# Kernel tuning notes

Hardware: AMD Instinct MI355X
Metric: run time of the kernel (lower is better)

Reference implementation:

```python
import jax, jax.numpy as jnp
import numpy as np

B, N, H, DQK, DV = 2, 2048, 16, 128, 128
E = H * DV
CHUNK = 64


def setup_inputs() -> dict:
    key = jax.random.key(0)
    ks = jax.random.split(key, 11)
    w = lambda k: jax.random.normal(k, (E, E), jnp.float32) * 0.02
    return {
        "x": jax.random.normal(ks[0], (B, N, E), jnp.float32),
        "prev_state": jnp.zeros((B, H, DQK, DV), jnp.float32),
        "Wq": w(ks[1]), "bq": jnp.zeros((E,), jnp.float32),
        "Wk": w(ks[2]), "bk": jnp.zeros((E,), jnp.float32),
        "Wv": w(ks[3]), "bv": jnp.zeros((E,), jnp.float32),
        "Wg": w(ks[4]), "bg": jnp.zeros((E,), jnp.float32),
        "Wo": w(ks[5]), "bo": jnp.zeros((E,), jnp.float32),
        "start_idx": 0,
    }


def _mul_i(t):
    # multiply interleaved complex pairs by i: (a, b) -> (-b, a)
    t2 = t.reshape(*t.shape[:-1], -1, 2)
    return jnp.stack((-t2[..., 1], t2[..., 0]), axis=-1).reshape(t.shape)


def reference(x, prev_state, Wq, bq, Wk, bk, Wv, bv, Wg, bg, Wo, bo, start_idx):
    b, n, e = x.shape
    h, dqk, dv, c = H, DQK, DV, CHUNK
    q = (x @ Wq.T + bq).reshape(b, n, h, dqk)
    k = (x @ Wk.T + bk).reshape(b, n, h, dqk)
    v = (x @ Wv.T + bv).reshape(b, n, h, dv)

    # xPos-style theta shift (rotary on interleaved pairs), applied along the sequence dim
    lin = jnp.linspace(0.0, 1.0, dqk // 2)
    thetas = jnp.repeat(1.0 / (10000.0 ** lin), 2).astype(x.dtype)  # (dqk,)
    idx = (start_idx + jnp.arange(n)).astype(x.dtype)
    ang = idx[:, None] * thetas[None, :]  # (n, dqk)
    sin = jnp.sin(ang)[None, :, None, :]
    cos = jnp.cos(ang)[None, :, None, :]
    q = q * cos + _mul_i(q) * sin
    k = k * cos + _mul_i(k) * sin
    k = k / jnp.sqrt(jnp.asarray(dqk, x.dtype))

    # per-head decays: 1 - 2^(-5 - h)
    gamma = 1.0 - jnp.exp2(-5.0 - jnp.arange(h, dtype=x.dtype))  # (h,)
    i = jnp.arange(c, dtype=x.dtype)
    mask = i[:, None] >= i[None, :]
    Dmat = jnp.where(mask, gamma[:, None, None] ** jnp.where(mask, i[:, None] - i[None, :], 0.0), 0.0)  # (h,c,c)
    cross_decay = gamma[:, None] ** (i[None, :] + 1.0)   # (h,c)
    kv_decay = gamma[:, None] ** (c - 1.0 - i[None, :])  # (h,c)
    chunk_decay = gamma ** c                              # (h,)

    nc = n // c
    qc = q.reshape(b, nc, c, h, dqk).transpose(1, 0, 3, 2, 4)  # (nc,b,h,c,dqk)
    kc = k.reshape(b, nc, c, h, dqk).transpose(1, 0, 3, 2, 4)
    vc = v.reshape(b, nc, c, h, dv).transpose(1, 0, 3, 2, 4)

    def step(S, qkv):
        qi, ki, vi = qkv  # (b,h,c,d)
        att = jnp.einsum('bhid,bhjd->bhij', qi, ki) * Dmat[None]
        o = jnp.einsum('bhij,bhje->bhie', att, vi)
        o = o + jnp.einsum('bhid,bhde->bhie', qi, S) * cross_decay[None, :, :, None]
        S_new = S * chunk_decay[None, :, None, None] + jnp.einsum('bhjd,bhje->bhde', ki * kv_decay[None, :, :, None], vi)
        return S_new, o

    state, outs = jax.lax.scan(step, prev_state, (qc, kc, vc))
    ret = outs.transpose(1, 0, 3, 2, 4).reshape(b, n, h, dv)

    # GroupNorm(num_groups=h, affine=False): normalize each head over dv
    mu = ret.mean(-1, keepdims=True)
    var = ((ret - mu) ** 2).mean(-1, keepdims=True)
    ret = ((ret - mu) / jnp.sqrt(var + 1e-6)).reshape(b, n, e)

    gate = jax.nn.silu(x @ Wg.T + bg)
    out = (ret * gate) @ Wo.T + bo
    return out, state
```

## Files before the change

kernel.cpp:

```cpp
#include <hip/hip_runtime.h>
#include <hip/hip_bf16.h>
#include <stdint.h>

#define B_   2
#define N_   2048
#define H_   16
#define DQK_ 128
#define DV_  128
#define E_   2048
#define CH_  64
#define NC_  32
#define M_   (B_*N_)
#define QKVG_LD 8192

using bf16x8 = __attribute__((ext_vector_type(8))) __bf16;
using f32x4  = __attribute__((ext_vector_type(4))) float;
typedef __hip_bfloat16 bf16_t;

__device__ __forceinline__ void gload_lds16(const void* g, void* l) {
  __builtin_amdgcn_global_load_lds(
      (const __attribute__((address_space(1))) void*)(uintptr_t)g,
      (__attribute__((address_space(3))) void*)(uint32_t)(uintptr_t)l,
      16, 0, 0);
}

__device__ __forceinline__ float head_log2g(int h) {
  return (float)(log2(1.0 - exp2((double)(-5 - h))));
}

__global__ void cvt_bf16_kernel(const float* __restrict__ src,
                                bf16_t* __restrict__ dst, int n4) {
  int i = blockIdx.x * 256 + threadIdx.x;
  if (i >= n4) return;
  float4 v = ((const float4*)src)[i];
  bf16_t o0 = __float2bfloat16(v.x), o1 = __float2bfloat16(v.y);
  bf16_t o2 = __float2bfloat16(v.z), o3 = __float2bfloat16(v.w);
  ushort4 p;
  p.x = *(unsigned short*)&o0; p.y = *(unsigned short*)&o1;
  p.z = *(unsigned short*)&o2; p.w = *(unsigned short*)&o3;
  ((ushort4*)dst)[i] = p;
}

template<bool OUT_BF16>
__global__ __launch_bounds__(512, 2)
void gemm8_kernel(const bf16_t* __restrict__ A, const bf16_t* __restrict__ Bw,
                  const float* __restrict__ bias, void* __restrict__ Cout,
                  int K, int ldc, int tilesM) {
  extern __shared__ char smem[];
  const int nwg = gridDim.x;
  const int bid = blockIdx.x;
  const int cpx = nwg >> 3;
  const int swz = (bid & 7) * cpx + (bid >> 3);
  const int tm = swz % tilesM, tn = swz / tilesM;
  const int rowT0 = tm * 256, colT0 = tn * 256;
  const int tid = threadIdx.x, wave = tid >> 6, lane = tid & 63;
  const int wr = wave >> 2, wc = wave & 3;
  const int l16 = lane & 15, lhi = lane >> 4;
  const int NKT = K >> 6;

  const int sw = ((tid & 7) * 16) ^ (((tid >> 3) & 7) << 4);
  const size_t aOff = (size_t)(rowT0 + (tid >> 3)) * K + (sw >> 1);
  const size_t bOff = (size_t)(colT0 + (tid >> 3)) * K + (sw >> 1);
  const uint32_t wl = wave * 1024;

  auto stage = [&](int h) {
    const int ktp = h >> 2, r = h & 3, buf = ktp & 1;
    const int k0 = ktp << 6;
    const int half = (r < 2) ? r : (r - 2);
    const bf16_t* src = (r < 2) ? Bw : A;
    const size_t off = (r < 2) ? bOff : aOff;
    const uint32_t base = ((r < 2) ? 65536u : 0u) + buf * 32768 + half * 16384 + wl;
#pragma unroll
    for (int L = 0; L < 2; L++)
      gload_lds16(src + off + (size_t)(half * 128 + L * 64) * K + k0,
                  smem + base + L * 8192);
  };

  for (int h = 0; h < 6; h++) stage(h);
  asm volatile("s_waitcnt vmcnt(4)" ::: "memory");
  __builtin_amdgcn_s_barrier();
  asm volatile("" ::: "memory");
  __builtin_amdgcn_sched_barrier(0);

  f32x4 acc[8][4] = {};
  bf16x8 bfr[4][2];

  for (int kt = 0; kt < NKT; kt++) {
    const int cur = kt & 1;
    const uint32_t aB = cur * 32768;
    const uint32_t bB = 65536 + cur * 32768;
#pragma unroll
    for (int p = 0; p < 4; p++) {
      bf16x8 afr[2][2];
      if (p == 0) {
#pragma unroll
        for (int n = 0; n < 4; n++) {
          const int r = wc * 64 + n * 16 + l16;
#pragma unroll
          for (int ks = 0; ks < 2; ks++) {
            const int cb = ks * 64 + lhi * 16;
            bfr[n][ks] = *(const bf16x8*)(smem + bB + r * 128 + (cb ^ ((r & 7) << 4)));
          }
        }
      }
#pragma unroll
      for (int mm = 0; mm < 2; mm++) {
        const int r = wr * 128 + p * 32 + mm * 16 + l16;
#pragma unroll
        for (int ks = 0; ks < 2; ks++) {
          const int cb = ks * 64 + lhi * 16;
          afr[mm][ks] = *(const bf16x8*)(smem + aB + r * 128 + (cb ^ ((r & 7) << 4)));
        }
      }
      const int h = 4 * kt + p + 6;
      if (h < 4 * NKT) stage(h);
      __builtin_amdgcn_s_barrier();
      asm volatile("s_waitcnt lgkmcnt(0)" ::: "memory");
      __builtin_amdgcn_sched_barrier(0);
      __builtin_amdgcn_s_setprio(1);
#pragma unroll
      for (int mm = 0; mm < 2; mm++)
#pragma unroll
        for (int n = 0; n < 4; n++)
#pragma unroll
          for (int ks = 0; ks < 2; ks++)
            acc[2 * p + mm][n] = __builtin_amdgcn_mfma_f32_16x16x32_bf16(
                afr[mm][ks], bfr[n][ks], acc[2 * p + mm][n], 0, 0, 0);
      __builtin_amdgcn_s_setprio(0);
      if (p == 3) {
        if (kt < NKT - 2)       asm volatile("s_waitcnt vmcnt(4)" ::: "memory");
        else if (kt == NKT - 2) asm volatile("s_waitcnt vmcnt(0)" ::: "memory");
      }
      __builtin_amdgcn_s_barrier();
      asm volatile("" ::: "memory");
      __builtin_amdgcn_sched_barrier(0);
    }
  }

#pragma unroll
  for (int m = 0; m < 8; m++) {
    const int rbase = rowT0 + wr * 128 + m * 16 + lhi * 4;
#pragma unroll
    for (int n = 0; n < 4; n++) {
      const int col = colT0 + wc * 64 + n * 16 + l16;
      const float bv = bias[col];
#pragma unroll
      for (int j = 0; j < 4; j++) {
        float v = acc[m][n][j] + bv;
        if (OUT_BF16) ((bf16_t*)Cout)[(size_t)(rbase + j) * ldc + col] = __float2bfloat16(v);
        else          ((float*)Cout)[(size_t)(rbase + j) * ldc + col] = v;
      }
    }
  }
}

__global__ void rotary_kernel(bf16_t* __restrict__ q, bf16_t* __restrict__ k,
                              const int* __restrict__ startp) {
  int t = blockIdx.x * 256 + threadIdx.x;
  if (t >= B_*N_*H_*16) return;
  int dg = t & 15;
  int rest = t >> 4;
  int n = (rest >> 4) & (N_ - 1);
  int h = rest & 15;
  float pos = (float)(startp[0] + n);
  size_t base = (size_t)(rest >> 4) * QKVG_LD + h * 128 + dg * 8;
  bf16x8 qv = *(const bf16x8*)(q + base);
  bf16x8 kv = *(const bf16x8*)(k + base);
  bf16x8 qo, ko;
  const float KS = 0.08838834764831843f;
#pragma unroll
  for (int p = 0; p < 4; p++) {
    int j = dg * 4 + p;
    float theta = exp2f(-13.287712379549449f * ((float)j * (1.0f/63.0f)));
    float ang = pos * theta;
    float s, c;
    sincosf(ang, &s, &c);
    float qa = (float)qv[2*p], qb = (float)qv[2*p+1];
    float ka = (float)kv[2*p], kb = (float)kv[2*p+1];
    qo[2*p]   = (__bf16)(qa*c - qb*s);
    qo[2*p+1] = (__bf16)(qb*c + qa*s);
    ko[2*p]   = (__bf16)((ka*c - kb*s) * KS);
    ko[2*p+1] = (__bf16)((kb*c + ka*s) * KS);
  }
  *(bf16x8*)(q + base) = qo;
  *(bf16x8*)(k + base) = ko;
}

__global__ __launch_bounds__(256)
void chunk_kvt_kernel(const bf16_t* __restrict__ kb, const bf16_t* __restrict__ vb,
                      bf16_t* __restrict__ kvt) {
  __shared__ alignas(16) char lds[32768];
  char* vts = lds;
  char* kts = lds + 16384;

  const int tid = threadIdx.x, wave = tid >> 6, lane = tid & 63;
  const int l16 = lane & 15, lhi = lane >> 4;
  const int blk = blockIdx.x;
  const int bh = blk >> 5, ch = blk & 31;
  const int h = bh & (H_ - 1);
  const float log2g = head_log2g(h);
  const int n0 = ch * 64;

  const size_t bhbase = (size_t)(bh >> 4) * N_ * QKVG_LD + (size_t)h * 128;

#pragma unroll
  for (int it = 0; it < 4; it++) {
    int j = it*16 + (tid >> 4);
    int e0 = (tid & 15) * 8;
    bf16x8 vv = *(const bf16x8*)(vb + bhbase + (size_t)(n0 + j)*QKVG_LD + e0);
    bf16x8 kk = *(const bf16x8*)(kb + bhbase + (size_t)(n0 + j)*QKVG_LD + e0);
    float kvd = exp2f((float)(63 - j) * log2g);
#pragma unroll
    for (int m = 0; m < 8; m++) {
      int e = e0 + m;
      *(__bf16*)(vts + e*128 + ((j*2) ^ ((e&7)<<4))) = vv[m];
      *(__bf16*)(kts + e*128 + ((j*2) ^ ((e&7)<<4))) = (__bf16)((float)kk[m] * kvd);
    }
  }
  __syncthreads();

  f32x4 acc[2][8] = {};
#pragma unroll
  for (int kk2 = 0; kk2 < 2; kk2++) {
#pragma unroll
    for (int et = 0; et < 2; et++) {
      int e = (2*wave + et)*16 + l16;
      bf16x8 vf = *(const bf16x8*)(vts + e*128 + (((kk2*32 + lhi*8)*2) ^ ((e&7)<<4)));
#pragma unroll
      for (int dt = 0; dt < 8; dt++) {
        int d = dt*16 + l16;
        bf16x8 kf = *(const bf16x8*)(kts + d*128 + (((kk2*32 + lhi*8)*2) ^ ((d&7)<<4)));
        acc[et][dt] = __builtin_amdgcn_mfma_f32_16x16x32_bf16(vf, kf, acc[et][dt], 0, 0, 0);
      }
    }
  }

  const size_t obase = (size_t)blk * 16384;
#pragma unroll
  for (int et = 0; et < 2; et++)
#pragma unroll
    for (int dt = 0; dt < 8; dt++)
#pragma unroll
      for (int j = 0; j < 4; j++) {
        int e = (2*wave + et)*16 + lhi*4 + j;
        int d = dt*16 + l16;
        kvt[obase + e*128 + d] = __float2bfloat16(acc[et][dt][j]);
      }
}

__global__ __launch_bounds__(256)
void state_scan_kernel(const bf16_t* __restrict__ kvt, const float* __restrict__ prev,
                       bf16_t* __restrict__ sbft, float* __restrict__ out_state) {
  int p = blockIdx.x * 256 + threadIdx.x;
  int bh = p >> 14;
  int ed = p & 16383;
  int e = ed >> 7, d = ed & 127;
  int h = bh & (H_ - 1);
  const float cdecay = exp2f(64.0f * head_log2g(h));

  float S = prev[(size_t)bh*16384 + d*128 + e];
  size_t boff = (size_t)bh * (NC_*16384) + ed;
  for (int ch = 0; ch < NC_; ch++) {
    sbft[boff] = __float2bfloat16(S);
    S = S * cdecay + __bfloat162float(kvt[boff]);
    boff += 16384;
  }
  out_state[(size_t)bh*16384 + d*128 + e] = S;
}

__global__ __launch_bounds__(256)
void chunk_out_kernel(const bf16_t* __restrict__ qb, const bf16_t* __restrict__ kb,
                      const bf16_t* __restrict__ vb, const bf16_t* __restrict__ sbft,
                      float* __restrict__ o_pre) {
  __shared__ alignas(16) char lds[24576];
  char* vts = lds;
  char* ats = lds + 16384;

  const int tid = threadIdx.x, wave = tid >> 6, lane = tid & 63;
  const int l16 = lane & 15, lhi = lane >> 4;
  const int blk = blockIdx.x;
  const int bh = blk >> 5, ch = blk & 31;
  const int h = bh & (H_ - 1);
  const float log2g = head_log2g(h);
  const int n0 = ch * 64;

  const size_t bhbase = (size_t)(bh >> 4) * N_ * QKVG_LD + (size_t)h * 128;
  const size_t obase_o = (size_t)(bh >> 4) * N_ * 2048 + (size_t)h * 128;
  const bf16_t* Srow = sbft + (size_t)blk * 16384;

#pragma unroll
  for (int it = 0; it < 4; it++) {
    int j = it*16 + (tid >> 4);
    int e0 = (tid & 15) * 8;
    bf16x8 vv = *(const bf16x8*)(vb + bhbase + (size_t)(n0 + j)*QKVG_LD + e0);
#pragma unroll
    for (int m = 0; m < 8; m++) {
      int e = e0 + m;
      *(__bf16*)(vts + e*128 + ((j*2) ^ ((e&7)<<4))) = vv[m];
    }
  }

  bf16x8 qf[4];
#pragma unroll
  for (int dk = 0; dk < 4; dk++)
    qf[dk] = *(const bf16x8*)(qb + bhbase + (size_t)(n0 + wave*16 + l16)*QKVG_LD + dk*32 + lhi*8);

  f32x4 aacc[4] = {};
#pragma unroll
  for (int jt = 0; jt < 4; jt++) {
#pragma unroll
    for (int dk = 0; dk < 4; dk++) {
      bf16x8 kf = *(const bf16x8*)(kb + bhbase + (size_t)(n0 + jt*16 + l16)*QKVG_LD + dk*32 + lhi*8);
      aacc[jt] = __builtin_amdgcn_mfma_f32_16x16x32_bf16(qf[dk], kf, aacc[jt], 0, 0, 0);
    }
  }
#pragma unroll
  for (int jt = 0; jt < 4; jt++)
#pragma unroll
    for (int j = 0; j < 4; j++) {
      int i = wave*16 + lhi*4 + j;
      int jc = jt*16 + l16;
      aacc[jt][j] *= (i >= jc) ? exp2f((float)(i - jc) * log2g) : 0.0f;
    }

#pragma unroll
  for (int jt = 0; jt < 4; jt++)
#pragma unroll
    for (int j = 0; j < 4; j++) {
      int i = wave*16 + lhi*4 + j;
      int jc = jt*16 + l16;
      *(__bf16*)(ats + i*128 + ((jc*2) ^ ((i&7)<<4))) = (__bf16)aacc[jt][j];
    }
  __syncthreads();

  f32x4 oacc[8] = {};
#pragma unroll
  for (int et = 0; et < 8; et++) {
#pragma unroll
    for (int dk = 0; dk < 4; dk++) {
      int e = et*16 + l16;
      bf16x8 sf = *(const bf16x8*)(Srow + e*128 + dk*32 + lhi*8);
      oacc[et] = __builtin_amdgcn_mfma_f32_16x16x32_bf16(qf[dk], sf, oacc[et], 0, 0, 0);
    }
  }
#pragma unroll
  for (int j = 0; j < 4; j++) {
    int i = wave*16 + lhi*4 + j;
    float f = exp2f((float)(i + 1) * log2g);
#pragma unroll
    for (int et = 0; et < 8; et++) oacc[et][j] *= f;
  }

#pragma unroll
  for (int kk2 = 0; kk2 < 2; kk2++) {
    int i = wave*16 + l16;
    bf16x8 af = *(const bf16x8*)(ats + i*128 + (((kk2*32 + lhi*8)*2) ^ ((i&7)<<4)));
#pragma unroll
    for (int et = 0; et < 8; et++) {
      int e = et*16 + l16;
      bf16x8 vf = *(const bf16x8*)(vts + e*128 + (((kk2*32 + lhi*8)*2) ^ ((e&7)<<4)));
      oacc[et] = __builtin_amdgcn_mfma_f32_16x16x32_bf16(af, vf, oacc[et], 0, 0, 0);
    }
  }

#pragma unroll
  for (int et = 0; et < 8; et++)
#pragma unroll
    for (int j = 0; j < 4; j++) {
      int i = wave*16 + lhi*4 + j;
      o_pre[obase_o + (size_t)(n0 + i)*2048 + et*16 + l16] = oacc[et][j];
    }
}

__global__ __launch_bounds__(256)
void gn_gate_kernel(const float* __restrict__ o_pre, const bf16_t* __restrict__ gbuf,
                    bf16_t* __restrict__ gated) {
  int row = blockIdx.x * 4 + (threadIdx.x >> 6);
  int lane = threadIdx.x & 63;
  size_t base = (size_t)row * 128 + lane * 2;
  size_t gbase = (size_t)(row >> 4) * QKVG_LD + (size_t)(row & 15) * 128 + lane * 2;
  float2 xv = *(const float2*)(o_pre + base);
  float s = xv.x + xv.y, ss = xv.x*xv.x + xv.y*xv.y;
#pragma unroll
  for (int off = 1; off < 64; off <<= 1) {
    s  += __shfl_xor(s, off);
    ss += __shfl_xor(ss, off);
  }
  float mu  = s * (1.0f/128.0f);
  float inv = rsqrtf(ss * (1.0f/128.0f) - mu*mu + 1e-6f);
  float g0 = __bfloat162float(gbuf[gbase]),  g1 = __bfloat162float(gbuf[gbase+1]);
  float r0 = (xv.x - mu) * inv * (g0 / (1.0f + expf(-g0)));
  float r1 = (xv.y - mu) * inv * (g1 / (1.0f + expf(-g1)));
  gated[base]   = __float2bfloat16(r0);
  gated[base+1] = __float2bfloat16(r1);
}

extern "C" void kernel_launch(void* const* d_in, const int* in_sizes, int n_in,
                              void* d_out, int out_size, void* d_ws, size_t ws_size,
                              hipStream_t stream) {
  const float* x    = (const float*)d_in[0];
  const float* prev = (const float*)d_in[1];
  const float* Wq = (const float*)d_in[2];  const float* bq = (const float*)d_in[3];
  const float* Wk = (const float*)d_in[4];  const float* bk = (const float*)d_in[5];
  const float* Wv = (const float*)d_in[6];  const float* bv = (const float*)d_in[7];
  const float* Wg = (const float*)d_in[8];  const float* bg = (const float*)d_in[9];
  const float* Wo = (const float*)d_in[10]; const float* bo = (const float*)d_in[11];
  const int* startp = (const int*)d_in[12];

  float* out = (float*)d_out;
  float* out_state = out + (size_t)B_*N_*E_;

  char* w = (char*)d_ws;
  const size_t XN = (size_t)B_*N_*E_;
  const size_t WN = (size_t)E_*E_;
  bf16_t* xb   = (bf16_t*)w;             w += XN*2;
  bf16_t* qkvg = (bf16_t*)w;             w += (size_t)M_*QKVG_LD*2;
  bf16_t* wob  = (bf16_t*)w;             w += WN*2;
  char*   wcat_region = w;               w += 4*WN*2;
  bf16_t* wcat = (bf16_t*)wcat_region;
  bf16_t* sbft = (bf16_t*)w;             w += (size_t)B_*H_*NC_*16384*2;
  bf16_t* kvt   = (bf16_t*)wcat_region;
  float*  o_pre = (float*)wcat_region;
  float*  bcat  = (float*)sbft;

  hipFuncSetAttribute(reinterpret_cast<const void*>(gemm8_kernel<true>),
                      hipFuncAttributeMaxDynamicSharedMemorySize, 131072);
  hipFuncSetAttribute(reinterpret_cast<const void*>(gemm8_kernel<false>),
                      hipFuncAttributeMaxDynamicSharedMemorySize, 131072);

  cvt_bf16_kernel<<<(int)(XN/4/256), 256, 0, stream>>>(x,  xb,  (int)(XN/4));
  cvt_bf16_kernel<<<(int)(WN/4/256), 256, 0, stream>>>(Wq, wcat,             (int)(WN/4));
  cvt_bf16_kernel<<<(int)(WN/4/256), 256, 0, stream>>>(Wk, wcat + WN,        (int)(WN/4));
  cvt_bf16_kernel<<<(int)(WN/4/256), 256, 0, stream>>>(Wv, wcat + 2*WN,      (int)(WN/4));
  cvt_bf16_kernel<<<(int)(WN/4/256), 256, 0, stream>>>(Wg, wcat + 3*WN,      (int)(WN/4));
  cvt_bf16_kernel<<<(int)(WN/4/256), 256, 0, stream>>>(Wo, wob, (int)(WN/4));

  hipMemcpyAsync(bcat,        bq, E_*4, hipMemcpyDeviceToDevice, stream);
  hipMemcpyAsync(bcat + E_,   bk, E_*4, hipMemcpyDeviceToDevice, stream);
  hipMemcpyAsync(bcat + 2*E_, bv, E_*4, hipMemcpyDeviceToDevice, stream);
  hipMemcpyAsync(bcat + 3*E_, bg, E_*4, hipMemcpyDeviceToDevice, stream);

  gemm8_kernel<true><<<512, 512, 131072, stream>>>(xb, wcat, bcat, (void*)qkvg,
                                                   E_, QKVG_LD, 16);

  rotary_kernel<<<(B_*N_*H_*16)/256, 256, 0, stream>>>(qkvg, qkvg + 2048, startp);

  chunk_kvt_kernel<<<B_*H_*NC_, 256, 0, stream>>>(qkvg + 2048, qkvg + 4096, kvt);
  state_scan_kernel<<<(B_*H_*16384)/256, 256, 0, stream>>>(kvt, prev, sbft, out_state);
  chunk_out_kernel<<<B_*H_*NC_, 256, 0, stream>>>(qkvg, qkvg + 2048, qkvg + 4096,
                                                  sbft, o_pre);

  gn_gate_kernel<<<(B_*N_*H_)/4, 256, 0, stream>>>(o_pre, qkvg + 6144, xb );

  gemm8_kernel<false><<<128, 512, 131072, stream>>>(xb, wob, bo, (void*)out,
                                                    E_, E_, 16);
}
```

Measured before the change: 325.5 us.

## Fuse conversions, fuse GroupNorm-gate into chunk output, narrow output GEMM tiles

All fp32-to-bf16 conversions and the bias copies are merged into a single launch, which removes six kernels and four memcpys. GroupNorm and the SiLU gate are fused into chunk_out_kernel through an LDS staging buffer, so the fp32 o_pre round trip through global memory is gone. The GEMM is templated on N-subtile count: the output projection uses 128-wide column tiles, giving 256 workgroups instead of 128 to fill more CUs. B fragments for the next k-tile are also prefetched early, with adjusted vmcnt waits. The risks are subtle errors in the hand-tuned waitcnt values and extra LDS use in the fused kernel.

```diff
diff --git a/kernel.cpp b/kernel.cpp
--- a/kernel.cpp
+++ b/kernel.cpp
@@ -28,20 +28,47 @@
   return (float)(log2(1.0 - exp2((double)(-5 - h))));
 }
 
-__global__ void cvt_bf16_kernel(const float* __restrict__ src,
-                                bf16_t* __restrict__ dst, int n4) {
-  int i = blockIdx.x * 256 + threadIdx.x;
-  if (i >= n4) return;
-  float4 v = ((const float4*)src)[i];
-  bf16_t o0 = __float2bfloat16(v.x), o1 = __float2bfloat16(v.y);
-  bf16_t o2 = __float2bfloat16(v.z), o3 = __float2bfloat16(v.w);
+__device__ __forceinline__ float bfu2f(unsigned short u) {
+  unsigned int t = (unsigned int)u << 16; float f;
+  __builtin_memcpy(&f, &t, 4); return f;
+}
+__device__ __forceinline__ unsigned short f2bfu(float f) {
+  bf16_t b = __float2bfloat16(f);
+  unsigned short u; __builtin_memcpy(&u, &b, 2); return u;
+}
+
+__global__ __launch_bounds__(256)
+void cvt_all_kernel(const float* __restrict__ x,
+                    const float* __restrict__ Wq, const float* __restrict__ Wk,
+                    const float* __restrict__ Wv, const float* __restrict__ Wg,
+                    const float* __restrict__ Wo,
+                    const float* __restrict__ bq, const float* __restrict__ bk,
+                    const float* __restrict__ bv, const float* __restrict__ bg,
+                    bf16_t* __restrict__ xb, bf16_t* __restrict__ wcat,
+                    bf16_t* __restrict__ wob, float* __restrict__ bcat) {
+  const int NX = 2097152, NW = 1048576;
+  int g = blockIdx.x * 256 + threadIdx.x;
+  const float* s; bf16_t* d; int si, di;
+  if (g < NX) { s = x; si = g; d = xb; di = g; }
+  else if (g < NX + 4*NW) {
+    int t = g - NX; int r = t / NW; si = t - r*NW;
+    s = (r==0) ? Wq : (r==1) ? Wk : (r==2) ? Wv : Wg; d = wcat; di = t;
+  } else if (g < NX + 5*NW) {
+    si = g - NX - 4*NW; s = Wo; d = wob; di = si;
+  } else {
+    int j = g - (NX + 5*NW);
+    int which = j >> 9, i = j & 511;
+    const float* bs = (which==0) ? bq : (which==1) ? bk : (which==2) ? bv : bg;
+    ((float4*)bcat)[which*512 + i] = ((const float4*)bs)[i];
+    return;
+  }
+  float4 v = ((const float4*)s)[si];
   ushort4 p;
-  p.x = *(unsigned short*)&o0; p.y = *(unsigned short*)&o1;
-  p.z = *(unsigned short*)&o2; p.w = *(unsigned short*)&o3;
-  ((ushort4*)dst)[i] = p;
-}
-
-template<bool OUT_BF16>
+  p.x = f2bfu(v.x); p.y = f2bfu(v.y); p.z = f2bfu(v.z); p.w = f2bfu(v.w);
+  ((ushort4*)d)[di] = p;
+}
+
+template<bool OUT_BF16, int NSUB>
 __global__ __launch_bounds__(512, 2)
 void gemm8_kernel(const bf16_t* __restrict__ A, const bf16_t* __restrict__ Bw,
                   const float* __restrict__ bias, void* __restrict__ Cout,
@@ -52,7 +79,7 @@
   const int cpx = nwg >> 3;
   const int swz = (bid & 7) * cpx + (bid >> 3);
   const int tm = swz % tilesM, tn = swz / tilesM;
-  const int rowT0 = tm * 256, colT0 = tn * 256;
+  const int rowT0 = tm * 256, colT0 = tn * (64 * NSUB);
   const int tid = threadIdx.x, wave = tid >> 6, lane = tid & 63;
   const int wr = wave >> 2, wc = wave & 3;
   const int l16 = lane & 15, lhi = lane >> 4;
@@ -66,43 +93,66 @@
   auto stage = [&](int h) {
     const int ktp = h >> 2, r = h & 3, buf = ktp & 1;
     const int k0 = ktp << 6;
-    const int half = (r < 2) ? r : (r - 2);
-    const bf16_t* src = (r < 2) ? Bw : A;
-    const size_t off = (r < 2) ? bOff : aOff;
-    const uint32_t base = ((r < 2) ? 65536u : 0u) + buf * 32768 + half * 16384 + wl;
-#pragma unroll
-    for (int L = 0; L < 2; L++)
-      gload_lds16(src + off + (size_t)(half * 128 + L * 64) * K + k0,
-                  smem + base + L * 8192);
+    if (r < 2) {
+      const uint32_t base = 65536u + buf * (8192u*NSUB) + r * (4096u*NSUB) + wl;
+#pragma unroll
+      for (int L = 0; L < NSUB/2; L++)
+        gload_lds16(Bw + bOff + (size_t)(r * (NSUB*32) + L * 64) * K + k0,
+                    smem + base + L * 8192);
+    } else {
+      const int half = r - 2;
+      const uint32_t base = buf * 32768u + half * 16384u + wl;
+#pragma unroll
+      for (int L = 0; L < 2; L++)
+        gload_lds16(A + aOff + (size_t)(half * 128 + L * 64) * K + k0,
+                    smem + base + L * 8192);
+    }
   };
 
   for (int h = 0; h < 6; h++) stage(h);
-  asm volatile("s_waitcnt vmcnt(4)" ::: "memory");
+  if constexpr (NSUB == 4) asm volatile("s_waitcnt vmcnt(4)" ::: "memory");
+  else                     asm volatile("s_waitcnt vmcnt(2)" ::: "memory");
   __builtin_amdgcn_s_barrier();
   asm volatile("" ::: "memory");
   __builtin_amdgcn_sched_barrier(0);
 
-  f32x4 acc[8][4] = {};
-  bf16x8 bfr[4][2];
+  f32x4 acc[8][NSUB] = {};
+  bf16x8 bfr[NSUB][2], bnx[2][2];
+
+#pragma unroll
+  for (int n = 0; n < 2; n++) {
+    const int r = wc * (16*NSUB) + n * 16 + l16;
+#pragma unroll
+    for (int ks = 0; ks < 2; ks++) {
+      const int cb = ks * 64 + lhi * 16;
+      bnx[n][ks] = *(const bf16x8*)(smem + 65536u + r * 128 + (cb ^ ((r & 7) << 4)));
+    }
+  }
 
   for (int kt = 0; kt < NKT; kt++) {
     const int cur = kt & 1;
-    const uint32_t aB = cur * 32768;
-    const uint32_t bB = 65536 + cur * 32768;
+    const uint32_t aB = cur * 32768u;
+    const uint32_t bB = 65536u + cur * (8192u*NSUB);
 #pragma unroll
     for (int p = 0; p < 4; p++) {
-      bf16x8 afr[2][2];
       if (p == 0) {
 #pragma unroll
-        for (int n = 0; n < 4; n++) {
-          const int r = wc * 64 + n * 16 + l16;
-#pragma unroll
-          for (int ks = 0; ks < 2; ks++) {
-            const int cb = ks * 64 + lhi * 16;
-            bfr[n][ks] = *(const bf16x8*)(smem + bB + r * 128 + (cb ^ ((r & 7) << 4)));
+        for (int n = 0; n < 2; n++)
+#pragma unroll
+          for (int ks = 0; ks < 2; ks++) bfr[n][ks] = bnx[n][ks];
+        if constexpr (NSUB == 4) {
+#pragma unroll
+          for (int n = 2; n < 4; n++) {
+            const int r = wc * (16*NSUB) + n * 16 + l16;
+#pragma unroll
+            for (int ks = 0; ks < 2; ks++) {
+              const int cb = ks * 64 + lhi * 16;
+              bfr[n][ks] = *(const bf16x8*)(smem + bB + r * 128 + (cb ^ ((r & 7) << 4)));
+            }
           }
         }
       }
+      bf16x8 afr[2][2];
 #pragma unroll
       for (int mm = 0; mm < 2; mm++) {
         const int r = wr * 128 + p * 32 + mm * 16 + l16;
@@ -121,15 +171,35 @@
 #pragma unroll
       for (int mm = 0; mm < 2; mm++)
 #pragma unroll
-        for (int n = 0; n < 4; n++)
+        for (int n = 0; n < NSUB; n++)
 #pragma unroll
           for (int ks = 0; ks < 2; ks++)
             acc[2 * p + mm][n] = __builtin_amdgcn_mfma_f32_16x16x32_bf16(
                 afr[mm][ks], bfr[n][ks], acc[2 * p + mm][n], 0, 0, 0);
       __builtin_amdgcn_s_setprio(0);
+      if (p == 2) {
+        if constexpr (NSUB == 4) asm volatile("s_waitcnt vmcnt(6)" ::: "memory");
+        else                     asm volatile("s_waitcnt vmcnt(5)" ::: "memory");
+      }
       if (p == 3) {
-        if (kt < NKT - 2)       asm volatile("s_waitcnt vmcnt(4)" ::: "memory");
-        else if (kt == NKT - 2) asm volatile("s_waitcnt vmcnt(0)" ::: "memory");
+        if (kt < NKT - 2) {
+          if constexpr (NSUB == 4) asm volatile("s_waitcnt vmcnt(4)" ::: "memory");
+          else                     asm volatile("s_waitcnt vmcnt(2)" ::: "memory");
+        } else if (kt == NKT - 2) {
+          asm volatile("s_waitcnt vmcnt(0)" ::: "memory");
+        }
+        if (kt + 1 < NKT) {
+          const uint32_t bN = 65536u + ((kt + 1) & 1) * (8192u*NSUB);
+#pragma unroll
+          for (int n = 0; n < 2; n++) {
+            const int r = wc * (16*NSUB) + n * 16 + l16;
+#pragma unroll
+            for (int ks = 0; ks < 2; ks++) {
+              const int cb = ks * 64 + lhi * 16;
+              bnx[n][ks] = *(const bf16x8*)(smem + bN + r * 128 + (cb ^ ((r & 7) << 4)));
+            }
+          }
+        }
       }
       __builtin_amdgcn_s_barrier();
       asm volatile("" ::: "memory");
@@ -141,8 +211,8 @@
   for (int m = 0; m < 8; m++) {
     const int rbase = rowT0 + wr * 128 + m * 16 + lhi * 4;
 #pragma unroll
-    for (int n = 0; n < 4; n++) {
-      const int col = colT0 + wc * 64 + n * 16 + l16;
+    for (int n = 0; n < NSUB; n++) {
+      const int col = colT0 + wc * (16*NSUB) + n * 16 + l16;
       const float bv = bias[col];
 #pragma unroll
       for (int j = 0; j < 4; j++) {
@@ -270,22 +340,23 @@
 
 __global__ __launch_bounds__(256)
 void chunk_out_kernel(const bf16_t* __restrict__ qb, const bf16_t* __restrict__ kb,
-                      const bf16_t* __restrict__ vb, const bf16_t* __restrict__ sbft,
-                      float* __restrict__ o_pre) {
-  __shared__ alignas(16) char lds[24576];
+                      const bf16_t* __restrict__ vb, const bf16_t* __restrict__ gb,
+                      const bf16_t* __restrict__ sbft, bf16_t* __restrict__ gated) {
+  __shared__ alignas(16) char lds[32768];
   char* vts = lds;
   char* ats = lds + 16384;
+  float* o_lds = (float*)lds;
 
   const int tid = threadIdx.x, wave = tid >> 6, lane = tid & 63;
   const int l16 = lane & 15, lhi = lane >> 4;
   const int blk = blockIdx.x;
   const int bh = blk >> 5, ch = blk & 31;
   const int h = bh & (H_ - 1);
+  const int b = bh >> 4;
   const float log2g = head_log2g(h);
   const int n0 = ch * 64;
 
-  const size_t bhbase = (size_t)(bh >> 4) * N_ * QKVG_LD + (size_t)h * 128;
-  const size_t obase_o = (size_t)(bh >> 4) * N_ * 2048 + (size_t)h * 128;
+  const size_t bhbase = (size_t)b * N_ * QKVG_LD + (size_t)h * 128;
   const bf16_t* Srow = sbft + (size_t)blk * 16384;
 
 #pragma unroll
@@ -363,36 +434,36 @@
     }
   }
 
+  __syncthreads();
 #pragma unroll
   for (int et = 0; et < 8; et++)
 #pragma unroll
     for (int j = 0; j < 4; j++) {
       int i = wave*16 + lhi*4 + j;
-      o_pre[obase_o + (size_t)(n0 + i)*2048 + et*16 + l16] = oacc[et][j];
-    }
-}
-
-__global__ __launch_bounds__(256)
-void gn_gate_kernel(const float* __restrict__ o_pre, const bf16_t* __restrict__ gbuf,
-                    bf16_t* __restrict__ gated) {
-  int row = blockIdx.x * 4 + (threadIdx.x >> 6);
-  int lane = threadIdx.x & 63;
-  size_t base = (size_t)row * 128 + lane * 2;
-  size_t gbase = (size_t)(row >> 4) * QKVG_LD + (size_t)(row & 15) * 128 + lane * 2;
-  float2 xv = *(const float2*)(o_pre + base);
-  float s = xv.x + xv.y, ss = xv.x*xv.x + xv.y*xv.y;
-#pragma unroll
-  for (int off = 1; off < 64; off <<= 1) {
-    s  += __shfl_xor(s, off);
-    ss += __shfl_xor(ss, off);
-  }
-  float mu  = s * (1.0f/128.0f);
-  float inv = rsqrtf(ss * (1.0f/128.0f) - mu*mu + 1e-6f);
-  float g0 = __bfloat162float(gbuf[gbase]),  g1 = __bfloat162float(gbuf[gbase+1]);
-  float r0 = (xv.x - mu) * inv * (g0 / (1.0f + expf(-g0)));
-  float r1 = (xv.y - mu) * inv * (g1 / (1.0f + expf(-g1)));
-  gated[base]   = __float2bfloat16(r0);
-  gated[base+1] = __float2bfloat16(r1);
+      o_lds[i*128 + et*16 + l16] = oacc[et][j];
+    }
+  __syncthreads();
+
+  for (int rr = 0; rr < 16; rr++) {
+    int r = wave*16 + rr;
+    float2 xv = *(const float2*)&o_lds[r*128 + lane*2];
+    float s = xv.x + xv.y, ss = xv.x*xv.x + xv.y*xv.y;
+#pragma unroll
+    for (int off = 1; off < 64; off <<= 1) {
+      s  += __shfl_xor(s, off);
+      ss += __shfl_xor(ss, off);
+    }
+    float mu  = s * (1.0f/128.0f);
+    float inv = rsqrtf(ss * (1.0f/128.0f) - mu*mu + 1e-6f);
+    size_t grow = (size_t)b * N_ + (n0 + r);
+    unsigned int gg = *(const unsigned int*)(gb + grow*QKVG_LD + h*128 + lane*2);
+    float g0 = bfu2f((unsigned short)(gg & 0xffff));
+    float g1 = bfu2f((unsigned short)(gg >> 16));
+    float r0 = (xv.x - mu) * inv * (g0 / (1.0f + expf(-g0)));
+    float r1 = (xv.y - mu) * inv * (g1 / (1.0f + expf(-g1)));
+    ushort2 o2; o2.x = f2bfu(r0); o2.y = f2bfu(r1);
+    *(ushort2*)(gated + grow*2048 + h*128 + lane*2) = o2;
+  }
 }
 
 extern "C" void kernel_launch(void* const* d_in, const int* in_sizes, int n_in,
@@ -420,38 +491,26 @@
   bf16_t* wcat = (bf16_t*)wcat_region;
   bf16_t* sbft = (bf16_t*)w;             w += (size_t)B_*H_*NC_*16384*2;
   bf16_t* kvt   = (bf16_t*)wcat_region;
-  float*  o_pre = (float*)wcat_region;
   float*  bcat  = (float*)sbft;
 
-  hipFuncSetAttribute(reinterpret_cast<const void*>(gemm8_kernel<true>),
+  hipFuncSetAttribute(reinterpret_cast<const void*>(gemm8_kernel<true,4>),
                       hipFuncAttributeMaxDynamicSharedMemorySize, 131072);
-  hipFuncSetAttribute(reinterpret_cast<const void*>(gemm8_kernel<false>),
-                      hipFuncAttributeMaxDynamicSharedMemorySize, 131072);
-
-  cvt_bf16_kernel<<<(int)(XN/4/256), 256, 0, stream>>>(x,  xb,  (int)(XN/4));
-  cvt_bf16_kernel<<<(int)(WN/4/256), 256, 0, stream>>>(Wq, wcat,             (int)(WN/4));
-  cvt_bf16_kernel<<<(int)(WN/4/256), 256, 0, stream>>>(Wk, wcat + WN,        (int)(WN/4));
-  cvt_bf16_kernel<<<(int)(WN/4/256), 256, 0, stream>>>(Wv, wcat + 2*WN,      (int)(WN/4));
-  cvt_bf16_kernel<<<(int)(WN/4/256), 256, 0, stream>>>(Wg, wcat + 3*WN,      (int)(WN/4));
-  cvt_bf16_kernel<<<(int)(WN/4/256), 256, 0, stream>>>(Wo, wob, (int)(WN/4));
-
-  hipMemcpyAsync(bcat,        bq, E_*4, hipMemcpyDeviceToDevice, stream);
-  hipMemcpyAsync(bcat + E_,   bk, E_*4, hipMemcpyDeviceToDevice, stream);
-  hipMemcpyAsync(bcat + 2*E_, bv, E_*4, hipMemcpyDeviceToDevice, stream);
-  hipMemcpyAsync(bcat + 3*E_, bg, E_*4, hipMemcpyDeviceToDevice, stream);
-
-  gemm8_kernel<true><<<512, 512, 131072, stream>>>(xb, wcat, bcat, (void*)qkvg,
-                                                   E_, QKVG_LD, 16);
+  hipFuncSetAttribute(reinterpret_cast<const void*>(gemm8_kernel<false,2>),
+                      hipFuncAttributeMaxDynamicSharedMemorySize, 98304);
+
+  cvt_all_kernel<<<28680, 256, 0, stream>>>(x, Wq, Wk, Wv, Wg, Wo, bq, bk, bv, bg,
+                                            xb, wcat, wob, bcat);
+
+  gemm8_kernel<true,4><<<512, 512, 131072, stream>>>(xb, wcat, bcat, (void*)qkvg,
+                                                     E_, QKVG_LD, 16);
 
   rotary_kernel<<<(B_*N_*H_*16)/256, 256, 0, stream>>>(qkvg, qkvg + 2048, startp);
 
   chunk_kvt_kernel<<<B_*H_*NC_, 256, 0, stream>>>(qkvg + 2048, qkvg + 4096, kvt);
   state_scan_kernel<<<(B_*H_*16384)/256, 256, 0, stream>>>(kvt, prev, sbft, out_state);
   chunk_out_kernel<<<B_*H_*NC_, 256, 0, stream>>>(qkvg, qkvg + 2048, qkvg + 4096,
-                                                  sbft, o_pre);
-
-  gn_gate_kernel<<<(B_*N_*H_)/4, 256, 0, stream>>>(o_pre, qkvg + 6144, xb );
-
-  gemm8_kernel<false><<<128, 512, 131072, stream>>>(xb, wob, bo, (void*)out,
-                                                    E_, E_, 16);
-}
+                                                  qkvg + 6144, sbft, xb );
+
+  gemm8_kernel<false,2><<<256, 512, 98304, stream>>>(xb, wob, bo, (void*)out,
+                                                     E_, E_, 16);
+}
```

Result: faster. 286.4 us (-12.0%).
